# Kernel optimization log

Hardware: AMD Instinct MI355X
Metric: run time of the kernel (lower is better)

The kernel has to match this reference:

```python
import jax, jax.numpy as jnp
import numpy as np

S, L, D = 128, 512, 256   # MSA rows, residues, msa_dim
H, C = 8, 32              # num_heads, head_dim


def setup_inputs() -> dict:
    key = jax.random.key(0)
    ks = jax.random.split(key, 8)
    inp = {
        "msa_input": jax.random.normal(ks[0], (S, L, D), dtype=jnp.float32),
        "ln_scale": jnp.ones((D,), jnp.float32),
        "ln_bias": jnp.zeros((D,), jnp.float32),
        "wq": jax.random.normal(ks[1], (D, H * C), jnp.float32) / np.sqrt(D),
        "wk": jax.random.normal(ks[2], (D, H * C), jnp.float32) / np.sqrt(D),
        "wv": jax.random.normal(ks[3], (D, H * C), jnp.float32) / np.sqrt(D),
        "wg": jax.random.normal(ks[4], (D, H * C), jnp.float32) / np.sqrt(D),
        "bg": jnp.zeros((H * C,), jnp.float32),
        "wo": jax.random.normal(ks[5], (H * C, D), jnp.float32) / np.sqrt(H * C),
        "bo": jnp.zeros((D,), jnp.float32),
    }
    return inp


def reference(msa_input, ln_scale, ln_bias, wq, wk, wv, wg, bg, wo, bo):
    # LayerNorm over last dim (eps matches torch default 1e-5)
    mu = jnp.mean(msa_input, axis=-1, keepdims=True)
    var = jnp.mean(jnp.square(msa_input - mu), axis=-1, keepdims=True)
    x = (msa_input - mu) * jax.lax.rsqrt(var + 1e-5) * ln_scale + ln_bias

    q = (x @ wq).reshape(S, L, H, C)
    k = (x @ wk).reshape(S, L, H, C)
    v = (x @ wv).reshape(S, L, H, C)
    g = jax.nn.sigmoid(x @ wg + bg).reshape(S, L, H, C)

    scale = 1.0 / np.sqrt(C)
    # attention over MSA-row axis, per residue l and head h
    scores = jnp.einsum("slhc,tlhc->stlh", q, k) * scale   # [S,S,L,H]
    probs = jax.nn.softmax(scores, axis=1)                  # softmax over t
    o = jnp.einsum("stlh,tlhc->slhc", probs, v) * g         # [S,L,H,C]
    return o.reshape(S, L, H * C) @ wo + bo
```

## Files before the change

### kernel.cpp

```cpp
#include <hip/hip_runtime.h>
#include <hip/hip_bf16.h>

typedef __bf16 bf16;
typedef __bf16 bf16x8 __attribute__((ext_vector_type(8)));
typedef float f32x4 __attribute__((ext_vector_type(4)));

#define S_DIM 128
#define L_DIM 512
#define D_DIM 256
#define NQ    1024

__device__ __forceinline__ void gl16(void* lds, const void* g) {
  __builtin_amdgcn_global_load_lds((const __attribute__((address_space(1))) void*)g,
                                   (__attribute__((address_space(3))) void*)lds,
                                   16, 0, 0);
}

__global__ void pack_weights(const float* __restrict__ wq, const float* __restrict__ wk,
                             const float* __restrict__ wv, const float* __restrict__ wg,
                             const float* __restrict__ wo,
                             bf16* __restrict__ wcat_t, bf16* __restrict__ wo_t) {
  int idx = blockIdx.x * 256 + threadIdx.x;
  const int total1 = NQ * D_DIM;
  if (idx < total1) {
    int j = idx >> 8;
    int d = idx & 255;
    const float* w = (j < 256) ? wq : (j < 512) ? wk : (j < 768) ? wv : wg;
    wcat_t[idx] = (bf16)w[d * 256 + (j & 255)];
  } else {
    int i2 = idx - total1;
    if (i2 < D_DIM * D_DIM) {
      int dcol = i2 >> 8, k = i2 & 255;
      wo_t[i2] = (bf16)wo[k * 256 + dcol];
    }
  }
}

__global__ __launch_bounds__(256) void ln_kernel(const float* __restrict__ x,
                                                 const float* __restrict__ sc,
                                                 const float* __restrict__ bs,
                                                 bf16* __restrict__ y) {
  int wid  = threadIdx.x >> 6;
  int lane = threadIdx.x & 63;
  int row  = blockIdx.x * 4 + wid;
  float4 v = ((const float4*)(x + (size_t)row * D_DIM))[lane];
  float s = v.x + v.y + v.z + v.w;
  #pragma unroll
  for (int m = 32; m; m >>= 1) s += __shfl_xor(s, m);
  float mu = s * (1.0f / 256.0f);
  float dx = v.x - mu, dy = v.y - mu, dz = v.z - mu, dw = v.w - mu;
  float s2 = dx * dx + dy * dy + dz * dz + dw * dw;
  #pragma unroll
  for (int m = 32; m; m >>= 1) s2 += __shfl_xor(s2, m);
  float rs = rsqrtf(s2 * (1.0f / 256.0f) + 1e-5f);
  float4 scv = ((const float4*)sc)[lane];
  float4 bsv = ((const float4*)bs)[lane];
  union { uint2 u; bf16 b[4]; } o;
  o.b[0] = (bf16)(dx * rs * scv.x + bsv.x);
  o.b[1] = (bf16)(dy * rs * scv.y + bsv.y);
  o.b[2] = (bf16)(dz * rs * scv.z + bsv.z);
  o.b[3] = (bf16)(dw * rs * scv.w + bsv.w);
  ((uint2*)y)[(size_t)row * 64 + lane] = o.u;
}

template <int MODE, int NCOLS, int NBBITS>
__global__ __launch_bounds__(256, 4) void gemm128(const bf16* __restrict__ A,
                                                  const bf16* __restrict__ Bt,
                                                  void* __restrict__ Cout,
                                                  const float* __restrict__ bias) {
  __shared__ __align__(16) bf16 smem[16384];
  bf16* As = smem;
  bf16* Bs = smem + 8192;
  const int tid  = threadIdx.x;
  const int wid  = tid >> 6;
  const int lane = tid & 63;
  const int bid   = blockIdx.x;
  const int n_idx = (bid >> 3) & ((1 << NBBITS) - 1);
  const int m_idx = (bid & 7) | ((bid >> (3 + NBBITS)) << 3);
  const int m0 = m_idx * 128;
  const int n0 = n_idx * 128;
  const int lrow = lane & 15;
  const int lk   = (lane >> 4) * 8;
  const int wr = wid >> 1, wc = wid & 1;

  const int ln8 = lane >> 3;
  const int c8  = (lane & 7) * 8;

  const bf16* Arow = A  + (size_t)m0 * 256 + c8;
  const bf16* Brow = Bt + (size_t)n0 * 256 + c8;

  f32x4 acc[4][4] = {};

  #pragma unroll
  for (int ks = 0; ks < 4; ++ks) {
    const int k0 = ks * 64;
    #pragma unroll
    for (int t = 0; t < 4; ++t) {
      int chunk = wid * 4 + t;
      int r = chunk * 8 + ln8;
      gl16(&As[chunk * 512], Arow + (size_t)r * 256 + k0);
      gl16(&Bs[chunk * 512], Brow + (size_t)r * 256 + k0);
    }
    __syncthreads();
    #pragma unroll
    for (int kk = 0; kk < 64; kk += 32) {
      bf16x8 av[4], bv[4];
      #pragma unroll
      for (int i = 0; i < 4; ++i)
        av[i] = *(const bf16x8*)(As + (wr * 64 + i * 16 + lrow) * 64 + kk + lk);
      #pragma unroll
      for (int j = 0; j < 4; ++j)
        bv[j] = *(const bf16x8*)(Bs + (wc * 64 + j * 16 + lrow) * 64 + kk + lk);
      #pragma unroll
      for (int i = 0; i < 4; ++i)
        #pragma unroll
        for (int j = 0; j < 4; ++j)
          acc[i][j] = __builtin_amdgcn_mfma_f32_16x16x32_bf16(av[i], bv[j], acc[i][j], 0, 0, 0);
    }
    __syncthreads();
  }

  const int rb = (lane >> 4) * 4;
  const int xorv = rb << 2;

  if (MODE == 0) {
    const bool isg = (n0 >= 768);
    float bgv[4];
    if (isg) {
      #pragma unroll
      for (int j = 0; j < 4; ++j) bgv[j] = bias[n0 - 768 + wc * 64 + j * 16 + lrow];
    }
    #pragma unroll
    for (int i = 0; i < 4; ++i)
      #pragma unroll
      for (int j = 0; j < 4; ++j) {
        int col = wc * 64 + j * 16 + lrow;
        #pragma unroll
        for (int r = 0; r < 4; ++r) {
          int row = wr * 64 + i * 16 + rb + r;
          float v = acc[i][j][r];
          if (isg) { v += bgv[j]; v = 1.0f / (1.0f + __expf(-v)); }
          smem[row * 128 + (col ^ xorv)] = (bf16)v;
        }
      }
    __syncthreads();
    #pragma unroll
    for (int p = 0; p < 8; ++p) {
      int chunk = p * 256 + tid;
      int row = chunk >> 4, slot8 = (chunk & 15) * 8;
      int rx = (row & 12) << 2;
      *(uint4*)((bf16*)Cout + (size_t)(m0 + row) * NCOLS + n0 + slot8) =
          *(const uint4*)(smem + row * 128 + (slot8 ^ rx));
    }
  } else {
    float* smf = (float*)smem;
    float bov[4];
    #pragma unroll
    for (int j = 0; j < 4; ++j) bov[j] = bias[n0 + wc * 64 + j * 16 + lrow];
    #pragma unroll
    for (int half = 0; half < 2; ++half) {
      if (half) __syncthreads();
      #pragma unroll
      for (int i2 = 0; i2 < 2; ++i2) {
        int i = half * 2 + i2;
        #pragma unroll
        for (int j = 0; j < 4; ++j) {
          int col = wc * 64 + j * 16 + lrow;
          #pragma unroll
          for (int r = 0; r < 4; ++r) {
            int crow = wr * 32 + i2 * 16 + rb + r;
            smf[crow * 128 + (col ^ xorv)] = acc[i][j][r] + bov[j];
          }
        }
      }
      __syncthreads();
      #pragma unroll
      for (int p = 0; p < 8; ++p) {
        int chunk = p * 256 + tid;
        int crow = chunk >> 5, slot = (chunk & 31) * 4;
        int rx = (crow & 12) << 2;
        int grow = m0 + (crow >> 5) * 64 + half * 32 + (crow & 31);
        *(uint4*)((float*)Cout + (size_t)grow * NCOLS + n0 + slot) =
            *(const uint4*)(smf + crow * 128 + (slot ^ rx));
      }
    }
  }
}

__global__ __launch_bounds__(256) void attn_kernel(const bf16* __restrict__ qkvg,
                                                   bf16* __restrict__ obuf) {
  __shared__ __align__(16) bf16 q_lds[128 * 40];
  __shared__ __align__(16) bf16 k_lds[128 * 40];
  __shared__ __align__(16) bf16 vt_lds[32 * 136];
  __shared__ __align__(16) bf16 p_lds[128 * 136];
  int bid = blockIdx.x;
  int h   = (bid >> 3) & 7;
  int res = (bid & 7) | ((bid >> 6) << 3);
  int tid = threadIdx.x;
  size_t base = (size_t)res * NQ + h * 32;

  for (int idx = tid; idx < 128 * 4; idx += 256) {
    int s = idx >> 2, c = (idx & 3) * 8;
    size_t g = (size_t)s * L_DIM * NQ + base + c;
    *(uint4*)(&q_lds[s * 40 + c]) = *(const uint4*)(qkvg + g);
    *(uint4*)(&k_lds[s * 40 + c]) = *(const uint4*)(qkvg + g + 256);
  }
  for (int idx = tid; idx < 128 * 4; idx += 256) {
    int t = idx >> 2, c = (idx & 3) * 8;
    union { uint4 u; bf16 e[8]; } v;
    v.u = *(const uint4*)(qkvg + (size_t)t * L_DIM * NQ + base + 512 + c);
    #pragma unroll
    for (int j = 0; j < 8; j++) vt_lds[(c + j) * 136 + t] = v.e[j];
  }
  __syncthreads();

  int wid = tid >> 6, lane = tid & 63;
  int lrow = lane & 15, lk = (lane >> 4) * 8;
  int s0 = wid * 32;

  f32x4 sc[2][8] = {};
  bf16x8 a0 = *(const bf16x8*)(&q_lds[(s0 + lrow) * 40 + lk]);
  bf16x8 a1 = *(const bf16x8*)(&q_lds[(s0 + 16 + lrow) * 40 + lk]);
  #pragma unroll
  for (int tc = 0; tc < 8; tc++) {
    bf16x8 b = *(const bf16x8*)(&k_lds[(tc * 16 + lrow) * 40 + lk]);
    sc[0][tc] = __builtin_amdgcn_mfma_f32_16x16x32_bf16(a0, b, sc[0][tc], 0, 0, 0);
    sc[1][tc] = __builtin_amdgcn_mfma_f32_16x16x32_bf16(a1, b, sc[1][tc], 0, 0, 0);
  }
  const float scale = 0.17677669529663687f;
  #pragma unroll
  for (int i = 0; i < 2; i++)
    #pragma unroll
    for (int tc = 0; tc < 8; tc++) sc[i][tc] *= scale;

  #pragma unroll
  for (int tr = 0; tr < 2; tr++)
    #pragma unroll
    for (int r = 0; r < 4; r++) {
      float m = -1e30f;
      #pragma unroll
      for (int tc = 0; tc < 8; tc++) m = fmaxf(m, sc[tr][tc][r]);
      #pragma unroll
      for (int msk = 8; msk; msk >>= 1) m = fmaxf(m, __shfl_xor(m, msk));
      float ssum = 0.f;
      #pragma unroll
      for (int tc = 0; tc < 8; tc++) {
        float p = __expf(sc[tr][tc][r] - m);
        sc[tr][tc][r] = p;
        ssum += p;
      }
      #pragma unroll
      for (int msk = 8; msk; msk >>= 1) ssum += __shfl_xor(ssum, msk);
      float inv = 1.0f / ssum;
      int prow = s0 + tr * 16 + (lane >> 4) * 4 + r;
      #pragma unroll
      for (int tc = 0; tc < 8; tc++)
        p_lds[prow * 136 + tc * 16 + lrow] = (bf16)(sc[tr][tc][r] * inv);
    }
  __syncthreads();

  f32x4 oc[2][2] = {};
  #pragma unroll
  for (int kc = 0; kc < 4; kc++) {
    bf16x8 pa0 = *(const bf16x8*)(&p_lds[(s0 + lrow) * 136 + kc * 32 + lk]);
    bf16x8 pa1 = *(const bf16x8*)(&p_lds[(s0 + 16 + lrow) * 136 + kc * 32 + lk]);
    bf16x8 b0  = *(const bf16x8*)(&vt_lds[lrow * 136 + kc * 32 + lk]);
    bf16x8 b1  = *(const bf16x8*)(&vt_lds[(16 + lrow) * 136 + kc * 32 + lk]);
    oc[0][0] = __builtin_amdgcn_mfma_f32_16x16x32_bf16(pa0, b0, oc[0][0], 0, 0, 0);
    oc[0][1] = __builtin_amdgcn_mfma_f32_16x16x32_bf16(pa0, b1, oc[0][1], 0, 0, 0);
    oc[1][0] = __builtin_amdgcn_mfma_f32_16x16x32_bf16(pa1, b0, oc[1][0], 0, 0, 0);
    oc[1][1] = __builtin_amdgcn_mfma_f32_16x16x32_bf16(pa1, b1, oc[1][1], 0, 0, 0);
  }

  int rbase = (lane >> 4) * 4;
  #pragma unroll
  for (int i = 0; i < 2; i++)
    #pragma unroll
    for (int j = 0; j < 2; j++)
      #pragma unroll
      for (int r = 0; r < 4; r++) {
        int srow = s0 + i * 16 + rbase + r;
        p_lds[srow * 136 + j * 16 + lrow] = (bf16)oc[i][j][r];
      }
  __syncthreads();

  #pragma unroll
  for (int p = 0; p < 2; p++) {
    int chunk = p * 256 + tid;
    int srow = chunk >> 2, slot = (chunk & 3) * 8;
    bf16x8 g8 = *(const bf16x8*)(qkvg + (size_t)srow * L_DIM * NQ + base + 768 + slot);
    bf16x8 o8 = *(const bf16x8*)(&p_lds[srow * 136 + slot]);
    bf16x8 r8;
    #pragma unroll
    for (int u = 0; u < 8; u++) r8[u] = (bf16)((float)o8[u] * (float)g8[u]);
    *(uint4*)(obuf + ((size_t)srow * L_DIM + res) * 256 + h * 32 + slot) = *(uint4*)&r8;
  }
}

extern "C" void kernel_launch(void* const* d_in, const int* in_sizes, int n_in,
                              void* d_out, int out_size, void* d_ws, size_t ws_size,
                              hipStream_t stream) {
  const float* msa      = (const float*)d_in[0];
  const float* ln_scale = (const float*)d_in[1];
  const float* ln_bias  = (const float*)d_in[2];
  const float* wq       = (const float*)d_in[3];
  const float* wk       = (const float*)d_in[4];
  const float* wv       = (const float*)d_in[5];
  const float* wg       = (const float*)d_in[6];
  const float* bg       = (const float*)d_in[7];
  const float* wo       = (const float*)d_in[8];
  const float* bo       = (const float*)d_in[9];
  float* out = (float*)d_out;

  char* ws = (char*)d_ws;
  bf16* wcat_t = (bf16*)ws;
  bf16* wo_t   = (bf16*)(ws + 524288);
  bf16* qkvg   = (bf16*)(ws + 655360);
  bf16* obuf   = (bf16*)(ws + 655360 + 134217728ULL);
  bf16* x_ln   = (bf16*)d_out;

  pack_weights<<<dim3(1280), dim3(256), 0, stream>>>(wq, wk, wv, wg, wo, wcat_t, wo_t);
  ln_kernel<<<dim3(65536 / 4), dim3(256), 0, stream>>>(msa, ln_scale, ln_bias, x_ln);
  gemm128<0, 1024, 3><<<dim3(4096), dim3(256), 0, stream>>>(x_ln, wcat_t, (void*)qkvg, bg);
  attn_kernel<<<dim3(4096), dim3(256), 0, stream>>>(qkvg, obuf);
  gemm128<1, 256, 1><<<dim3(1024), dim3(256), 0, stream>>>(obuf, wo_t, (void*)out, bo);
}
```

Before: 166.1 us.

## Fuse attention with output projection per residue and swizzle GEMM LDS

Replaces the separate attention kernel and output-projection GEMM with one kernel. Each block owns one residue, loops over the 8 heads, and accumulates the gated attention output times Wo in registers. This removes the 32MB obuf round trip through HBM and one launch. The QKVG GEMM also gets an XOR-swizzled LDS layout to avoid bank conflicts on its fragment reads. In exchange, the grid shrinks to 512 blocks of 512 threads, and the kernel adds per-head serialization and syncs. It also uses strided gathers of qkvg rows across S.

```diff
diff --git a/kernel.cpp b/kernel.cpp
--- a/kernel.cpp
+++ b/kernel.cpp
@@ -63,11 +63,14 @@
   ((uint2*)y)[(size_t)row * 64 + lane] = o.u;
 }
 
-template <int MODE, int NCOLS, int NBBITS>
-__global__ __launch_bounds__(256, 4) void gemm128(const bf16* __restrict__ A,
-                                                  const bf16* __restrict__ Bt,
-                                                  void* __restrict__ Cout,
-                                                  const float* __restrict__ bias) {
+__device__ __forceinline__ bf16x8 lds_swz(const bf16* base, int row, int k) {
+  return *(const bf16x8*)((const char*)base + ((((row << 6) + k) << 1) ^ ((row & 7) << 4)));
+}
+
+__global__ __launch_bounds__(256, 4) void gemm_qkvg(const bf16* __restrict__ A,
+                                                    const bf16* __restrict__ Bt,
+                                                    bf16* __restrict__ Cout,
+                                                    const float* __restrict__ bias) {
   __shared__ __align__(16) bf16 smem[16384];
   bf16* As = smem;
   bf16* Bs = smem + 8192;
@@ -75,8 +78,8 @@
   const int wid  = tid >> 6;
   const int lane = tid & 63;
   const int bid   = blockIdx.x;
-  const int n_idx = (bid >> 3) & ((1 << NBBITS) - 1);
-  const int m_idx = (bid & 7) | ((bid >> (3 + NBBITS)) << 3);
+  const int n_idx = (bid >> 3) & 7;
+  const int m_idx = (bid & 7) | ((bid >> 6) << 3);
   const int m0 = m_idx * 128;
   const int n0 = n_idx * 128;
   const int lrow = lane & 15;
@@ -84,7 +87,7 @@
   const int wr = wid >> 1, wc = wid & 1;
 
   const int ln8 = lane >> 3;
-  const int c8  = (lane & 7) * 8;
+  const int c8  = ((lane & 7) ^ ln8) * 8;
 
   const bf16* Arow = A  + (size_t)m0 * 256 + c8;
   const bf16* Brow = Bt + (size_t)n0 * 256 + c8;
@@ -107,10 +110,10 @@
       bf16x8 av[4], bv[4];
       #pragma unroll
       for (int i = 0; i < 4; ++i)
-        av[i] = *(const bf16x8*)(As + (wr * 64 + i * 16 + lrow) * 64 + kk + lk);
+        av[i] = lds_swz(As, wr * 64 + i * 16 + lrow, kk + lk);
       #pragma unroll
       for (int j = 0; j < 4; ++j)
-        bv[j] = *(const bf16x8*)(Bs + (wc * 64 + j * 16 + lrow) * 64 + kk + lk);
+        bv[j] = lds_swz(Bs, wc * 64 + j * 16 + lrow, kk + lk);
       #pragma unroll
       for (int i = 0; i < 4; ++i)
         #pragma unroll
@@ -123,177 +126,186 @@
   const int rb = (lane >> 4) * 4;
   const int xorv = rb << 2;
 
-  if (MODE == 0) {
-    const bool isg = (n0 >= 768);
-    float bgv[4];
-    if (isg) {
-      #pragma unroll
-      for (int j = 0; j < 4; ++j) bgv[j] = bias[n0 - 768 + wc * 64 + j * 16 + lrow];
-    }
-    #pragma unroll
-    for (int i = 0; i < 4; ++i)
-      #pragma unroll
-      for (int j = 0; j < 4; ++j) {
-        int col = wc * 64 + j * 16 + lrow;
+  const bool isg = (n0 >= 768);
+  float bgv[4];
+  if (isg) {
+    #pragma unroll
+    for (int j = 0; j < 4; ++j) bgv[j] = bias[n0 - 768 + wc * 64 + j * 16 + lrow];
+  }
+  #pragma unroll
+  for (int i = 0; i < 4; ++i)
+    #pragma unroll
+    for (int j = 0; j < 4; ++j) {
+      int col = wc * 64 + j * 16 + lrow;
+      #pragma unroll
+      for (int r = 0; r < 4; ++r) {
+        int row = wr * 64 + i * 16 + rb + r;
+        float v = acc[i][j][r];
+        if (isg) { v += bgv[j]; v = 1.0f / (1.0f + __expf(-v)); }
+        smem[row * 128 + (col ^ xorv)] = (bf16)v;
+      }
+    }
+  __syncthreads();
+  #pragma unroll
+  for (int p = 0; p < 8; ++p) {
+    int chunk = p * 256 + tid;
+    int row = chunk >> 4, slot8 = (chunk & 15) * 8;
+    int rx = (row & 12) << 2;
+    *(uint4*)(Cout + (size_t)(m0 + row) * NQ + n0 + slot8) =
+        *(const uint4*)(smem + row * 128 + (slot8 ^ rx));
+  }
+}
+
+__global__ __launch_bounds__(512) void attn_proj(const bf16* __restrict__ qkvg,
+                                                 const bf16* __restrict__ wo_t,
+                                                 const float* __restrict__ bo,
+                                                 float* __restrict__ out) {
+  __shared__ __align__(16) bf16 q_s[128 * 32];
+  __shared__ __align__(16) bf16 k_s[128 * 32];
+  __shared__ __align__(16) bf16 vt_s[32 * 136];
+  __shared__ __align__(16) char p_rg[34816];
+  bf16*  p_s = (bf16*)p_rg;
+  bf16*  w_s = (bf16*)p_rg;
+  float* f_b = (float*)p_rg;
+
+  const int tid  = threadIdx.x;
+  const int wid  = tid >> 6;
+  const int lane = tid & 63;
+  const int lrow = lane & 15;
+  const int lk   = (lane >> 4) * 8;
+  const int rb   = (lane >> 4) * 4;
+  const int res  = blockIdx.x;
+
+  const int wm = wid >> 1;
+  const int wn = wid & 1;
+  const int s0 = wid * 16;
+
+  float bov[8];
+  #pragma unroll
+  for (int j = 0; j < 8; ++j) bov[j] = bo[wn * 128 + j * 16 + lrow];
+
+  f32x4 acc[2][8] = {};
+
+  const int srow = (wid * 64 + lane) >> 2;
+  const int sslot = lane & 3;
+
+  for (int h = 0; h < 8; ++h) {
+    const int hc0 = h * 32;
+    {
+      const bf16* src = qkvg + ((size_t)srow * L_DIM + res) * NQ + hc0 + sslot * 8;
+      gl16(q_s + wid * 512, src);
+      gl16(k_s + wid * 512, src + 256);
+      int row = tid >> 2, slot = tid & 3;
+      union { uint4 u; bf16 e[8]; } v;
+      v.u = *(const uint4*)(qkvg + ((size_t)row * L_DIM + res) * NQ + 512 + hc0 + slot * 8);
+      #pragma unroll
+      for (int j = 0; j < 8; ++j) vt_s[(slot * 8 + j) * 136 + row] = v.e[j];
+    }
+    __syncthreads();
+
+    f32x4 s8[8];
+    {
+      const f32x4 z = {0.f, 0.f, 0.f, 0.f};
+      bf16x8 av = *(const bf16x8*)(q_s + (s0 + lrow) * 32 + lk);
+      #pragma unroll
+      for (int tc = 0; tc < 8; ++tc) {
+        bf16x8 bv = *(const bf16x8*)(k_s + (tc * 16 + lrow) * 32 + lk);
+        s8[tc] = __builtin_amdgcn_mfma_f32_16x16x32_bf16(av, bv, z, 0, 0, 0);
+      }
+    }
+    const float scale = 0.17677669529663687f;
+    #pragma unroll
+    for (int r = 0; r < 4; ++r) {
+      float m = -1e30f;
+      #pragma unroll
+      for (int tc = 0; tc < 8; ++tc) m = fmaxf(m, s8[tc][r]);
+      #pragma unroll
+      for (int msk = 8; msk; msk >>= 1) m = fmaxf(m, __shfl_xor(m, msk));
+      float pv[8], ssum = 0.f;
+      #pragma unroll
+      for (int tc = 0; tc < 8; ++tc) {
+        float p = __expf((s8[tc][r] - m) * scale);
+        pv[tc] = p; ssum += p;
+      }
+      #pragma unroll
+      for (int msk = 8; msk; msk >>= 1) ssum += __shfl_xor(ssum, msk);
+      float inv = 1.0f / ssum;
+      int prow = s0 + rb + r;
+      #pragma unroll
+      for (int tc = 0; tc < 8; ++tc)
+        p_s[prow * 136 + tc * 16 + lrow] = (bf16)(pv[tc] * inv);
+    }
+
+    f32x4 oc[2] = {};
+    #pragma unroll
+    for (int kc = 0; kc < 4; ++kc) {
+      bf16x8 pa = *(const bf16x8*)(p_s + (s0 + lrow) * 136 + kc * 32 + lk);
+      bf16x8 b0 = *(const bf16x8*)(vt_s + lrow * 136 + kc * 32 + lk);
+      bf16x8 b1 = *(const bf16x8*)(vt_s + (16 + lrow) * 136 + kc * 32 + lk);
+      oc[0] = __builtin_amdgcn_mfma_f32_16x16x32_bf16(pa, b0, oc[0], 0, 0, 0);
+      oc[1] = __builtin_amdgcn_mfma_f32_16x16x32_bf16(pa, b1, oc[1], 0, 0, 0);
+    }
+    #pragma unroll
+    for (int cj = 0; cj < 2; ++cj)
+      #pragma unroll
+      for (int r = 0; r < 4; ++r)
+        q_s[(s0 + rb + r) * 32 + cj * 16 + lrow] = (bf16)oc[cj][r];
+    __syncthreads();
+
+    #pragma unroll
+    for (int t = 0; t < 2; ++t) {
+      int ch = t * 512 + wid * 64 + lane;
+      int row = ch >> 2, slot = ch & 3;
+      gl16((char*)p_rg + (t * 512 + wid * 64) * 16, wo_t + row * 256 + hc0 + slot * 8);
+    }
+    {
+      int row = tid >> 2, slot = tid & 3;
+      union { uint4 u; bf16 e[8]; } g, o;
+      g.u = *(const uint4*)(qkvg + ((size_t)row * L_DIM + res) * NQ + 768 + hc0 + slot * 8);
+      o.u = *(const uint4*)(q_s + row * 32 + slot * 8);
+      #pragma unroll
+      for (int j = 0; j < 8; ++j) o.e[j] = (bf16)((float)o.e[j] * (float)g.e[j]);
+      *(uint4*)(q_s + row * 32 + slot * 8) = o.u;
+    }
+    __syncthreads();
+
+    {
+      bf16x8 av0 = *(const bf16x8*)(q_s + (wm * 32 + lrow) * 32 + lk);
+      bf16x8 av1 = *(const bf16x8*)(q_s + (wm * 32 + 16 + lrow) * 32 + lk);
+      #pragma unroll
+      for (int j = 0; j < 8; ++j) {
+        bf16x8 bv = *(const bf16x8*)(w_s + (wn * 128 + j * 16 + lrow) * 32 + lk);
+        acc[0][j] = __builtin_amdgcn_mfma_f32_16x16x32_bf16(av0, bv, acc[0][j], 0, 0, 0);
+        acc[1][j] = __builtin_amdgcn_mfma_f32_16x16x32_bf16(av1, bv, acc[1][j], 0, 0, 0);
+      }
+    }
+    __syncthreads();
+  }
+
+  #pragma unroll 1
+  for (int b = 0; b < 4; ++b) {
+    if (wm == b) {
+      #pragma unroll
+      for (int i = 0; i < 2; ++i)
         #pragma unroll
-        for (int r = 0; r < 4; ++r) {
-          int row = wr * 64 + i * 16 + rb + r;
-          float v = acc[i][j][r];
-          if (isg) { v += bgv[j]; v = 1.0f / (1.0f + __expf(-v)); }
-          smem[row * 128 + (col ^ xorv)] = (bf16)v;
-        }
-      }
-    __syncthreads();
-    #pragma unroll
-    for (int p = 0; p < 8; ++p) {
-      int chunk = p * 256 + tid;
-      int row = chunk >> 4, slot8 = (chunk & 15) * 8;
-      int rx = (row & 12) << 2;
-      *(uint4*)((bf16*)Cout + (size_t)(m0 + row) * NCOLS + n0 + slot8) =
-          *(const uint4*)(smem + row * 128 + (slot8 ^ rx));
-    }
-  } else {
-    float* smf = (float*)smem;
-    float bov[4];
-    #pragma unroll
-    for (int j = 0; j < 4; ++j) bov[j] = bias[n0 + wc * 64 + j * 16 + lrow];
-    #pragma unroll
-    for (int half = 0; half < 2; ++half) {
-      if (half) __syncthreads();
-      #pragma unroll
-      for (int i2 = 0; i2 < 2; ++i2) {
-        int i = half * 2 + i2;
-        #pragma unroll
-        for (int j = 0; j < 4; ++j) {
-          int col = wc * 64 + j * 16 + lrow;
+        for (int j = 0; j < 8; ++j)
           #pragma unroll
           for (int r = 0; r < 4; ++r) {
-            int crow = wr * 32 + i2 * 16 + rb + r;
-            smf[crow * 128 + (col ^ xorv)] = acc[i][j][r] + bov[j];
+            int br = i * 16 + rb + r;
+            int col = wn * 128 + j * 16 + lrow;
+            f_b[br * 256 + (col ^ ((br & 12) << 2))] = acc[i][j][r] + bov[j];
           }
-        }
-      }
-      __syncthreads();
-      #pragma unroll
-      for (int p = 0; p < 8; ++p) {
-        int chunk = p * 256 + tid;
-        int crow = chunk >> 5, slot = (chunk & 31) * 4;
-        int rx = (crow & 12) << 2;
-        int grow = m0 + (crow >> 5) * 64 + half * 32 + (crow & 31);
-        *(uint4*)((float*)Cout + (size_t)grow * NCOLS + n0 + slot) =
-            *(const uint4*)(smf + crow * 128 + (slot ^ rx));
-      }
-    }
-  }
-}
-
-__global__ __launch_bounds__(256) void attn_kernel(const bf16* __restrict__ qkvg,
-                                                   bf16* __restrict__ obuf) {
-  __shared__ __align__(16) bf16 q_lds[128 * 40];
-  __shared__ __align__(16) bf16 k_lds[128 * 40];
-  __shared__ __align__(16) bf16 vt_lds[32 * 136];
-  __shared__ __align__(16) bf16 p_lds[128 * 136];
-  int bid = blockIdx.x;
-  int h   = (bid >> 3) & 7;
-  int res = (bid & 7) | ((bid >> 6) << 3);
-  int tid = threadIdx.x;
-  size_t base = (size_t)res * NQ + h * 32;
-
-  for (int idx = tid; idx < 128 * 4; idx += 256) {
-    int s = idx >> 2, c = (idx & 3) * 8;
-    size_t g = (size_t)s * L_DIM * NQ + base + c;
-    *(uint4*)(&q_lds[s * 40 + c]) = *(const uint4*)(qkvg + g);
-    *(uint4*)(&k_lds[s * 40 + c]) = *(const uint4*)(qkvg + g + 256);
-  }
-  for (int idx = tid; idx < 128 * 4; idx += 256) {
-    int t = idx >> 2, c = (idx & 3) * 8;
-    union { uint4 u; bf16 e[8]; } v;
-    v.u = *(const uint4*)(qkvg + (size_t)t * L_DIM * NQ + base + 512 + c);
-    #pragma unroll
-    for (int j = 0; j < 8; j++) vt_lds[(c + j) * 136 + t] = v.e[j];
-  }
-  __syncthreads();
-
-  int wid = tid >> 6, lane = tid & 63;
-  int lrow = lane & 15, lk = (lane >> 4) * 8;
-  int s0 = wid * 32;
-
-  f32x4 sc[2][8] = {};
-  bf16x8 a0 = *(const bf16x8*)(&q_lds[(s0 + lrow) * 40 + lk]);
-  bf16x8 a1 = *(const bf16x8*)(&q_lds[(s0 + 16 + lrow) * 40 + lk]);
-  #pragma unroll
-  for (int tc = 0; tc < 8; tc++) {
-    bf16x8 b = *(const bf16x8*)(&k_lds[(tc * 16 + lrow) * 40 + lk]);
-    sc[0][tc] = __builtin_amdgcn_mfma_f32_16x16x32_bf16(a0, b, sc[0][tc], 0, 0, 0);
-    sc[1][tc] = __builtin_amdgcn_mfma_f32_16x16x32_bf16(a1, b, sc[1][tc], 0, 0, 0);
-  }
-  const float scale = 0.17677669529663687f;
-  #pragma unroll
-  for (int i = 0; i < 2; i++)
-    #pragma unroll
-    for (int tc = 0; tc < 8; tc++) sc[i][tc] *= scale;
-
-  #pragma unroll
-  for (int tr = 0; tr < 2; tr++)
-    #pragma unroll
-    for (int r = 0; r < 4; r++) {
-      float m = -1e30f;
-      #pragma unroll
-      for (int tc = 0; tc < 8; tc++) m = fmaxf(m, sc[tr][tc][r]);
-      #pragma unroll
-      for (int msk = 8; msk; msk >>= 1) m = fmaxf(m, __shfl_xor(m, msk));
-      float ssum = 0.f;
-      #pragma unroll
-      for (int tc = 0; tc < 8; tc++) {
-        float p = __expf(sc[tr][tc][r] - m);
-        sc[tr][tc][r] = p;
-        ssum += p;
-      }
-      #pragma unroll
-      for (int msk = 8; msk; msk >>= 1) ssum += __shfl_xor(ssum, msk);
-      float inv = 1.0f / ssum;
-      int prow = s0 + tr * 16 + (lane >> 4) * 4 + r;
-      #pragma unroll
-      for (int tc = 0; tc < 8; tc++)
-        p_lds[prow * 136 + tc * 16 + lrow] = (bf16)(sc[tr][tc][r] * inv);
-    }
-  __syncthreads();
-
-  f32x4 oc[2][2] = {};
-  #pragma unroll
-  for (int kc = 0; kc < 4; kc++) {
-    bf16x8 pa0 = *(const bf16x8*)(&p_lds[(s0 + lrow) * 136 + kc * 32 + lk]);
-    bf16x8 pa1 = *(const bf16x8*)(&p_lds[(s0 + 16 + lrow) * 136 + kc * 32 + lk]);
-    bf16x8 b0  = *(const bf16x8*)(&vt_lds[lrow * 136 + kc * 32 + lk]);
-    bf16x8 b1  = *(const bf16x8*)(&vt_lds[(16 + lrow) * 136 + kc * 32 + lk]);
-    oc[0][0] = __builtin_amdgcn_mfma_f32_16x16x32_bf16(pa0, b0, oc[0][0], 0, 0, 0);
-    oc[0][1] = __builtin_amdgcn_mfma_f32_16x16x32_bf16(pa0, b1, oc[0][1], 0, 0, 0);
-    oc[1][0] = __builtin_amdgcn_mfma_f32_16x16x32_bf16(pa1, b0, oc[1][0], 0, 0, 0);
-    oc[1][1] = __builtin_amdgcn_mfma_f32_16x16x32_bf16(pa1, b1, oc[1][1], 0, 0, 0);
-  }
-
-  int rbase = (lane >> 4) * 4;
-  #pragma unroll
-  for (int i = 0; i < 2; i++)
-    #pragma unroll
-    for (int j = 0; j < 2; j++)
-      #pragma unroll
-      for (int r = 0; r < 4; r++) {
-        int srow = s0 + i * 16 + rbase + r;
-        p_lds[srow * 136 + j * 16 + lrow] = (bf16)oc[i][j][r];
-      }
-  __syncthreads();
-
-  #pragma unroll
-  for (int p = 0; p < 2; p++) {
-    int chunk = p * 256 + tid;
-    int srow = chunk >> 2, slot = (chunk & 3) * 8;
-    bf16x8 g8 = *(const bf16x8*)(qkvg + (size_t)srow * L_DIM * NQ + base + 768 + slot);
-    bf16x8 o8 = *(const bf16x8*)(&p_lds[srow * 136 + slot]);
-    bf16x8 r8;
-    #pragma unroll
-    for (int u = 0; u < 8; u++) r8[u] = (bf16)((float)o8[u] * (float)g8[u]);
-    *(uint4*)(obuf + ((size_t)srow * L_DIM + res) * 256 + h * 32 + slot) = *(uint4*)&r8;
+    }
+    __syncthreads();
+    #pragma unroll
+    for (int u = 0; u < 4; ++u) {
+      int ch = u * 512 + tid;
+      int br = ch >> 6, slot = ch & 63;
+      int phys = (slot * 4) ^ ((br & 12) << 2);
+      *(uint4*)(out + ((size_t)(b * 32 + br) * L_DIM + res) * 256 + slot * 4) =
+          *(const uint4*)(f_b + br * 256 + phys);
+    }
+    __syncthreads();
   }
 }
 
@@ -316,12 +328,10 @@
   bf16* wcat_t = (bf16*)ws;
   bf16* wo_t   = (bf16*)(ws + 524288);
   bf16* qkvg   = (bf16*)(ws + 655360);
-  bf16* obuf   = (bf16*)(ws + 655360 + 134217728ULL);
   bf16* x_ln   = (bf16*)d_out;
 
   pack_weights<<<dim3(1280), dim3(256), 0, stream>>>(wq, wk, wv, wg, wo, wcat_t, wo_t);
   ln_kernel<<<dim3(65536 / 4), dim3(256), 0, stream>>>(msa, ln_scale, ln_bias, x_ln);
-  gemm128<0, 1024, 3><<<dim3(4096), dim3(256), 0, stream>>>(x_ln, wcat_t, (void*)qkvg, bg);
-  attn_kernel<<<dim3(4096), dim3(256), 0, stream>>>(qkvg, obuf);
-  gemm128<1, 256, 1><<<dim3(1024), dim3(256), 0, stream>>>(obuf, wo_t, (void*)out, bo);
-}
+  gemm_qkvg<<<dim3(4096), dim3(256), 0, stream>>>(x_ln, wcat_t, qkvg, bg);
+  attn_proj<<<dim3(512), dim3(512), 0, stream>>>(qkvg, wo_t, bo, out);
+}
```

After: 164.4 us. No clear change (-1.0%).
